# Kernel optimization log

Hardware: AMD Instinct MI355X
Metric: run time of the kernel (lower is better)

## Reference

```python
import jax, jax.numpy as jnp
import numpy as np

BATCH = 1048576
D_IN = 4        # d_in=3 spatial dims + 1 time dim
HID = 64
N_HID_STACK = 4  # hidden residual blocks after the first hidden layer
D_OUT = 3
BN_EPS = 1e-5


def _bn(x, gamma, beta):
    # BatchNorm1d in training mode: biased batch statistics over the batch axis
    mu = jnp.mean(x, axis=0)
    var = jnp.var(x, axis=0)
    return gamma * (x - mu) * jax.lax.rsqrt(var + BN_EPS) + beta


def setup_inputs() -> dict:
    key = jax.random.key(0)
    ks = jax.random.split(key, 8)
    s_in = 1.0 / np.sqrt(D_IN)
    s_h = 1.0 / np.sqrt(HID)
    return {
        "x": jax.random.normal(ks[0], (BATCH, D_IN), dtype=jnp.float32),
        "bn0_gamma": jnp.ones((D_IN,), jnp.float32),
        "bn0_beta": jnp.zeros((D_IN,), jnp.float32),
        "W0": jax.random.normal(ks[1], (D_IN, HID), jnp.float32) * s_in,
        "b0": jnp.zeros((HID,), jnp.float32),
        "gamma0": jnp.ones((HID,), jnp.float32),
        "beta0": jnp.zeros((HID,), jnp.float32),
        "W_hid": jax.random.normal(ks[2], (N_HID_STACK, HID, HID), jnp.float32) * s_h,
        "b_hid": jnp.zeros((N_HID_STACK, HID), jnp.float32),
        "gamma_hid": jnp.ones((N_HID_STACK, HID), jnp.float32),
        "beta_hid": jnp.zeros((N_HID_STACK, HID), jnp.float32),
        "Wout": jax.random.normal(ks[3], (HID, D_OUT), jnp.float32) * s_h,
        "bout": jnp.zeros((D_OUT,), jnp.float32),
    }


def reference(x, bn0_gamma, bn0_beta, W0, b0, gamma0, beta0,
              W_hid, b_hid, gamma_hid, beta_hid, Wout, bout):
    # Net.forward (u-network, single patch, batch_normalization=True, tanh):
    #   x = bn0(x)
    #   y = bn(act(Linear0(x)))                 (first hidden layer, no skip)
    #   y = bn_i(act(Linear_i(y))) + y          (residual hidden layers)
    #   y = Linear_out(y)
    h = _bn(x, bn0_gamma, bn0_beta)
    y = _bn(jnp.tanh(h @ W0 + b0), gamma0, beta0)

    def step(y, layer):
        W, b, g, be = layer
        return _bn(jnp.tanh(y @ W + b), g, be) + y, None

    y, _ = jax.lax.scan(step, y, (W_hid, b_hid, gamma_hid, beta_hid))
    return y @ Wout + bout
```

## Files before the change

### kernel.cpp

```cpp
#include <hip/hip_runtime.h>
#include <stdint.h>


#define NROWS 1048576
#define EPS 1e-5f
#define INV_B 9.5367431640625e-07f
#define LOG2E2 2.885390081777927f
#define BIGGRID 16384

typedef __attribute__((ext_vector_type(8))) short bfrag;
typedef __attribute__((ext_vector_type(4))) float facc;
typedef __attribute__((ext_vector_type(4))) float f4v;

__device__ __forceinline__ float bf2f(short s) {
  union { unsigned u; float f; } v;
  v.u = ((unsigned)(unsigned short)s) << 16;
  return v.f;
}
__device__ __forceinline__ short f2bf(float f) {
  union { float f; unsigned u; } v;
  v.f = f;
  unsigned r = v.u + 0x7FFFu + ((v.u >> 16) & 1u);
  return (short)(r >> 16);
}
__device__ __forceinline__ float tanh_fast(float x) {
  float e = __builtin_amdgcn_exp2f(x * LOG2E2);
  return 1.f - 2.f * __builtin_amdgcn_rcpf(e + 1.f);
}

template <int W>
__global__ __launch_bounds__(256) void k_reduce(const float* __restrict__ P,
                                                float* __restrict__ S,
                                                int rows_per_blk) {
  __shared__ float red[256];
  const int tid = threadIdx.x;
  const int col = tid % W;
  const int grp = tid / W;
  const int G = 256 / W;
  size_t r0 = (size_t)blockIdx.x * rows_per_blk;
  float s = 0.f;
  for (int r = grp; r < rows_per_blk; r += G) s += P[(r0 + r) * W + col];
  red[tid] = s;
  __syncthreads();
  if (tid < W) {
    float t = 0.f;
#pragma unroll 4
    for (int g = 0; g < G; ++g) t += red[g * W + tid];
    atomicAdd(&S[tid], t);
  }
}


__global__ __launch_bounds__(256) void k_stats_x(const float* __restrict__ x,
                                                 float* __restrict__ P) {
  __shared__ float red[4][8];
  const int tid = threadIdx.x;
  const int wave = tid >> 6;
  size_t base = (size_t)blockIdx.x * 1024 + tid;
  float s[4] = {0.f, 0.f, 0.f, 0.f}, q[4] = {0.f, 0.f, 0.f, 0.f};
#pragma unroll
  for (int it = 0; it < 4; ++it) {
    f4v v = *(const f4v*)(x + (base + (size_t)it * 256) * 4);
#pragma unroll
    for (int k = 0; k < 4; ++k) { s[k] += v[k]; q[k] = fmaf(v[k], v[k], q[k]); }
  }
#pragma unroll
  for (int off = 32; off > 0; off >>= 1) {
#pragma unroll
    for (int k = 0; k < 4; ++k) {
      s[k] += __shfl_xor(s[k], off);
      q[k] += __shfl_xor(q[k], off);
    }
  }
  if ((tid & 63) == 0) {
#pragma unroll
    for (int k = 0; k < 4; ++k) { red[wave][k] = s[k]; red[wave][4 + k] = q[k]; }
  }
  __syncthreads();
  if (tid < 8)
    P[blockIdx.x * 8 + tid] =
        red[0][tid] + red[1][tid] + red[2][tid] + red[3][tid];
}

__global__ __launch_bounds__(256) void k_stats_z1(
    const float* __restrict__ x, const float* __restrict__ bn0g,
    const float* __restrict__ bn0b, const float* __restrict__ W0,
    const float* __restrict__ b0, const float* __restrict__ sx,
    float* __restrict__ P) {
  __shared__ float red[2][4][64];
  const int tid = threadIdx.x;
  const int lane = tid & 63;
  const int wave = tid >> 6;
  int gw = blockIdx.x * 4 + wave;
  float sc[4], sh[4];
#pragma unroll
  for (int k = 0; k < 4; ++k) {
    float mean = sx[k] * INV_B;
    float var = fmaf(-mean, mean, sx[4 + k] * INV_B);
    float rs = rsqrtf(var + EPS);
    sc[k] = bn0g[k] * rs;
    sh[k] = fmaf(-sc[k], mean, bn0b[k]);
  }
  float w[4];
#pragma unroll
  for (int k = 0; k < 4; ++k) w[k] = W0[k * 64 + lane];
  float bj = b0[lane];
  float s = 0.f, q = 0.f;
  size_t r0 = (size_t)gw * 256;
  for (int r = 0; r < 256; ++r) {
    f4v xv = *(const f4v*)(x + (r0 + r) * 4);
    float acc = bj;
#pragma unroll
    for (int k = 0; k < 4; ++k)
      acc = fmaf(fmaf(xv[k], sc[k], sh[k]), w[k], acc);
    float z = tanh_fast(acc);
    s += z;
    q = fmaf(z, z, q);
  }
  red[0][wave][lane] = s;
  red[1][wave][lane] = q;
  __syncthreads();
  if (tid < 128) {
    int which = tid >> 6, c = tid & 63;
    P[blockIdx.x * 128 + tid] = red[which][0][c] + red[which][1][c] +
                                red[which][2][c] + red[which][3][c];
  }
}

__global__ __launch_bounds__(256) void k_prep(const float* __restrict__ Wh,
                                              short* __restrict__ WT) {
  int idx = blockIdx.x * 256 + threadIdx.x;
  int l = idx >> 12, rem = idx & 4095, k = rem >> 6, c = rem & 63;
  WT[l * 4096 + c * 64 + k] = f2bf(Wh[l * 4096 + k * 64 + c]);
}


__global__ __launch_bounds__(128) void k_first(
    const float* __restrict__ x, const float* __restrict__ bn0g,
    const float* __restrict__ bn0b, const float* __restrict__ W0,
    const float* __restrict__ b0, const float* __restrict__ gamma0,
    const float* __restrict__ beta0, const float* __restrict__ sx,
    const float* __restrict__ s1, const short* __restrict__ WTb,
    const float* __restrict__ bb, float* __restrict__ P,
    short* __restrict__ Y) {
  __shared__ __align__(16) float lds_x[64 * 4];
  __shared__ __align__(16) short lds_y[64 * 72];
  __shared__ float lds_st[128];

  const int tid = threadIdx.x;
  const int lane = tid & 63;
  const int wave = tid >> 6;
  const int l15 = lane & 15;
  const int q = lane >> 4;
  const int wr = wave * 32;
  const size_t r0 = (size_t)blockIdx.x * 64;

  f4v xp;
  if (lane < 32) xp = *(const f4v*)(x + (r0 + wr + lane) * 4);

  lds_st[tid] = 0.f;
  float sc0[4], sh0[4];
#pragma unroll
  for (int k = 0; k < 4; ++k) {
    float mean = sx[k] * INV_B;
    float var = fmaf(-mean, mean, sx[4 + k] * INV_B);
    float rs = rsqrtf(var + EPS);
    sc0[k] = bn0g[k] * rs;
    sh0[k] = fmaf(-sc0[k], mean, bn0b[k]);
  }
  float w0c[4];
#pragma unroll
  for (int k = 0; k < 4; ++k) w0c[k] = W0[k * 64 + lane];
  float b0c = b0[lane];
  float mean1 = s1[lane] * INV_B;
  float var1 = fmaf(-mean1, mean1, s1[64 + lane] * INV_B);
  float A1c = gamma0[lane] * rsqrtf(var1 + EPS);
  float B1c = fmaf(-A1c, mean1, beta0[lane]);
  if (lane < 32) *(f4v*)&lds_x[(wr + lane) * 4] = xp;
  __syncthreads();

  for (int e = 0; e < 32; ++e) {
    int row = wr + e;
    float acc = b0c;
#pragma unroll
    for (int k = 0; k < 4; ++k)
      acc = fmaf(fmaf(lds_x[row * 4 + k], sc0[k], sh0[k]), w0c[k], acc);
    float z = tanh_fast(acc);
    lds_y[row * 72 + lane] = f2bf(fmaf(A1c, z, B1c));
  }

  bfrag af[2][2];
#pragma unroll
  for (int mt = 0; mt < 2; ++mt)
#pragma unroll
    for (int kt = 0; kt < 2; ++kt) {
      af[mt][kt] =
          *(const bfrag*)&lds_y[(wr + mt * 16 + l15) * 72 + kt * 32 + q * 8];
      *(bfrag*)(Y + (r0 + wr + mt * 16 + l15) * 64 + kt * 32 + q * 8) =
          af[mt][kt];
    }
  float bbv[4];
  bfrag bwb[4][2];
#pragma unroll
  for (int nt = 0; nt < 4; ++nt) {
    bbv[nt] = bb[nt * 16 + l15];
#pragma unroll
    for (int kt = 0; kt < 2; ++kt)
      bwb[nt][kt] =
          *(const bfrag*)(WTb + (nt * 16 + l15) * 64 + kt * 32 + q * 8);
  }
  facc acc2[2][4];
#pragma unroll
  for (int mt = 0; mt < 2; ++mt)
#pragma unroll
    for (int nt = 0; nt < 4; ++nt) {
      acc2[mt][nt][0] = bbv[nt]; acc2[mt][nt][1] = bbv[nt];
      acc2[mt][nt][2] = bbv[nt]; acc2[mt][nt][3] = bbv[nt];
    }
#pragma unroll
  for (int mt = 0; mt < 2; ++mt)
#pragma unroll
    for (int nt = 0; nt < 4; ++nt)
#pragma unroll
      for (int kt = 0; kt < 2; ++kt)
        acc2[mt][nt] = __builtin_amdgcn_mfma_f32_16x16x32_bf16(
            af[mt][kt], bwb[nt][kt], acc2[mt][nt], 0, 0, 0);
  float sAcc[4], qAcc[4];
#pragma unroll
  for (int nt = 0; nt < 4; ++nt) {
    sAcc[nt] = 0.f;
    qAcc[nt] = 0.f;
#pragma unroll
    for (int mt = 0; mt < 2; ++mt)
#pragma unroll
      for (int i = 0; i < 4; ++i) {
        float z = tanh_fast(acc2[mt][nt][i]);
        sAcc[nt] += z;
        qAcc[nt] = fmaf(z, z, qAcc[nt]);
      }
    float s = sAcc[nt], ss = qAcc[nt];
    s += __shfl_xor(s, 16); s += __shfl_xor(s, 32);
    ss += __shfl_xor(ss, 16); ss += __shfl_xor(ss, 32);
    if (q == 0) {
      atomicAdd(&lds_st[nt * 16 + l15], s);
      atomicAdd(&lds_st[64 + nt * 16 + l15], ss);
    }
  }
  __syncthreads();
  P[(size_t)blockIdx.x * 128 + tid] = lds_st[tid];
}

__global__ __launch_bounds__(128) void k_mid(
    short* __restrict__ Y, const short* __restrict__ WTa,
    const float* __restrict__ ba, const float* __restrict__ ga,
    const float* __restrict__ bea, const float* __restrict__ sa,
    const short* __restrict__ WTb, const float* __restrict__ bb,
    float* __restrict__ P) {
  __shared__ __align__(16) short lds_y[64 * 72];
  __shared__ float lds_st[128];

  const int tid = threadIdx.x;
  const int lane = tid & 63;
  const int wave = tid >> 6;
  const int l15 = lane & 15;
  const int q = lane >> 4;
  const int wr = wave * 32;
  const size_t r0 = (size_t)blockIdx.x * 64;
  const int srow = lane >> 3;
  const int sc8 = (lane & 7) * 8;

  bfrag ld[4];
  {
    const size_t g = (r0 + wr + srow) * 64 + sc8;
#pragma unroll
    for (int it = 0; it < 4; ++it)
      ld[it] = *(const bfrag*)(Y + g + (size_t)it * 8 * 64);
  }

  lds_st[tid] = 0.f;
  float Av[4], Bv[4], bav[4];
#pragma unroll
  for (int nt = 0; nt < 4; ++nt) {
    int c = nt * 16 + l15;
    float mean = sa[c] * INV_B;
    float var = fmaf(-mean, mean, sa[64 + c] * INV_B);
    float A = ga[c] * rsqrtf(var + EPS);
    Av[nt] = A;
    Bv[nt] = fmaf(-A, mean, bea[c]);
    bav[nt] = ba[c];
  }
  bfrag bwa[4][2];
#pragma unroll
  for (int nt = 0; nt < 4; ++nt)
#pragma unroll
    for (int kt = 0; kt < 2; ++kt)
      bwa[nt][kt] =
          *(const bfrag*)(WTa + (nt * 16 + l15) * 64 + kt * 32 + q * 8);

#pragma unroll
  for (int it = 0; it < 4; ++it)
    *(bfrag*)&lds_y[(wr + it * 8 + srow) * 72 + sc8] = ld[it];
  __syncthreads();

  bfrag af[2][2];
#pragma unroll
  for (int mt = 0; mt < 2; ++mt)
#pragma unroll
    for (int kt = 0; kt < 2; ++kt)
      af[mt][kt] =
          *(const bfrag*)&lds_y[(wr + mt * 16 + l15) * 72 + kt * 32 + q * 8];
  facc acc[2][4];
#pragma unroll
  for (int mt = 0; mt < 2; ++mt)
#pragma unroll
    for (int nt = 0; nt < 4; ++nt) {
      acc[mt][nt][0] = bav[nt]; acc[mt][nt][1] = bav[nt];
      acc[mt][nt][2] = bav[nt]; acc[mt][nt][3] = bav[nt];
    }
#pragma unroll
  for (int mt = 0; mt < 2; ++mt)
#pragma unroll
    for (int nt = 0; nt < 4; ++nt)
#pragma unroll
      for (int kt = 0; kt < 2; ++kt)
        acc[mt][nt] = __builtin_amdgcn_mfma_f32_16x16x32_bf16(
            af[mt][kt], bwa[nt][kt], acc[mt][nt], 0, 0, 0);

#pragma unroll
  for (int mt = 0; mt < 2; ++mt)
#pragma unroll
    for (int nt = 0; nt < 4; ++nt) {
      int c = nt * 16 + l15;
      float A = Av[nt], Bc = Bv[nt];
#pragma unroll
      for (int i = 0; i < 4; ++i) {
        int rl = wr + mt * 16 + q * 4 + i;
        float z = tanh_fast(acc[mt][nt][i]);
        float yo = bf2f(lds_y[rl * 72 + c]);
        lds_y[rl * 72 + c] = f2bf(fmaf(A, z, Bc) + yo);
      }
    }

#pragma unroll
  for (int mt = 0; mt < 2; ++mt)
#pragma unroll
    for (int kt = 0; kt < 2; ++kt) {
      af[mt][kt] =
          *(const bfrag*)&lds_y[(wr + mt * 16 + l15) * 72 + kt * 32 + q * 8];
      *(bfrag*)(Y + (r0 + wr + mt * 16 + l15) * 64 + kt * 32 + q * 8) =
          af[mt][kt];
    }
  float bbv[4];
  bfrag bwb[4][2];
#pragma unroll
  for (int nt = 0; nt < 4; ++nt) {
    bbv[nt] = bb[nt * 16 + l15];
#pragma unroll
    for (int kt = 0; kt < 2; ++kt)
      bwb[nt][kt] =
          *(const bfrag*)(WTb + (nt * 16 + l15) * 64 + kt * 32 + q * 8);
  }
#pragma unroll
  for (int mt = 0; mt < 2; ++mt)
#pragma unroll
    for (int nt = 0; nt < 4; ++nt) {
      acc[mt][nt][0] = bbv[nt]; acc[mt][nt][1] = bbv[nt];
      acc[mt][nt][2] = bbv[nt]; acc[mt][nt][3] = bbv[nt];
    }
#pragma unroll
  for (int mt = 0; mt < 2; ++mt)
#pragma unroll
    for (int nt = 0; nt < 4; ++nt)
#pragma unroll
      for (int kt = 0; kt < 2; ++kt)
        acc[mt][nt] = __builtin_amdgcn_mfma_f32_16x16x32_bf16(
            af[mt][kt], bwb[nt][kt], acc[mt][nt], 0, 0, 0);
#pragma unroll
  for (int nt = 0; nt < 4; ++nt) {
    float s = 0.f, ss = 0.f;
#pragma unroll
    for (int mt = 0; mt < 2; ++mt)
#pragma unroll
      for (int i = 0; i < 4; ++i) {
        float z = tanh_fast(acc[mt][nt][i]);
        s += z;
        ss = fmaf(z, z, ss);
      }
    s += __shfl_xor(s, 16); s += __shfl_xor(s, 32);
    ss += __shfl_xor(ss, 16); ss += __shfl_xor(ss, 32);
    if (q == 0) {
      atomicAdd(&lds_st[nt * 16 + l15], s);
      atomicAdd(&lds_st[64 + nt * 16 + l15], ss);
    }
  }
  __syncthreads();
  P[(size_t)blockIdx.x * 128 + tid] = lds_st[tid];
}

__global__ __launch_bounds__(128) void k_last(
    const short* __restrict__ Y, const short* __restrict__ WTa,
    const float* __restrict__ ba, const float* __restrict__ ga,
    const float* __restrict__ bea, const float* __restrict__ sa,
    const float* __restrict__ Wout, const float* __restrict__ bout,
    float* __restrict__ out) {
  __shared__ __align__(16) short lds_y[64 * 72];
  __shared__ float lds_wo[192];

  const int tid = threadIdx.x;
  const int lane = tid & 63;
  const int wave = tid >> 6;
  const int l15 = lane & 15;
  const int q = lane >> 4;
  const int wr = wave * 32;
  const size_t r0 = (size_t)blockIdx.x * 64;
  const int srow = lane >> 3;
  const int sc8 = (lane & 7) * 8;

  bfrag ld[4];
  {
    const size_t g = (r0 + wr + srow) * 64 + sc8;
#pragma unroll
    for (int it = 0; it < 4; ++it)
      ld[it] = *(const bfrag*)(Y + g + (size_t)it * 8 * 64);
  }

  for (int i = tid; i < 192; i += 128) lds_wo[i] = Wout[i];
  float Av[4], Bv[4], bav[4];
#pragma unroll
  for (int nt = 0; nt < 4; ++nt) {
    int c = nt * 16 + l15;
    float mean = sa[c] * INV_B;
    float var = fmaf(-mean, mean, sa[64 + c] * INV_B);
    float A = ga[c] * rsqrtf(var + EPS);
    Av[nt] = A;
    Bv[nt] = fmaf(-A, mean, bea[c]);
    bav[nt] = ba[c];
  }
  bfrag bwa[4][2];
#pragma unroll
  for (int nt = 0; nt < 4; ++nt)
#pragma unroll
    for (int kt = 0; kt < 2; ++kt)
      bwa[nt][kt] =
          *(const bfrag*)(WTa + (nt * 16 + l15) * 64 + kt * 32 + q * 8);
  float bo0 = bout[0], bo1 = bout[1], bo2 = bout[2];

#pragma unroll
  for (int it = 0; it < 4; ++it)
    *(bfrag*)&lds_y[(wr + it * 8 + srow) * 72 + sc8] = ld[it];
  __syncthreads();

  bfrag af[2][2];
#pragma unroll
  for (int mt = 0; mt < 2; ++mt)
#pragma unroll
    for (int kt = 0; kt < 2; ++kt)
      af[mt][kt] =
          *(const bfrag*)&lds_y[(wr + mt * 16 + l15) * 72 + kt * 32 + q * 8];
  facc acc[2][4];
#pragma unroll
  for (int mt = 0; mt < 2; ++mt)
#pragma unroll
    for (int nt = 0; nt < 4; ++nt) {
      acc[mt][nt][0] = bav[nt]; acc[mt][nt][1] = bav[nt];
      acc[mt][nt][2] = bav[nt]; acc[mt][nt][3] = bav[nt];
    }
#pragma unroll
  for (int mt = 0; mt < 2; ++mt)
#pragma unroll
    for (int nt = 0; nt < 4; ++nt)
#pragma unroll
      for (int kt = 0; kt < 2; ++kt)
        acc[mt][nt] = __builtin_amdgcn_mfma_f32_16x16x32_bf16(
            af[mt][kt], bwa[nt][kt], acc[mt][nt], 0, 0, 0);
#pragma unroll
  for (int mt = 0; mt < 2; ++mt)
#pragma unroll
    for (int nt = 0; nt < 4; ++nt) {
      int c = nt * 16 + l15;
      float A = Av[nt], Bc = Bv[nt];
#pragma unroll
      for (int i = 0; i < 4; ++i) {
        int rl = wr + mt * 16 + q * 4 + i;
        float z = tanh_fast(acc[mt][nt][i]);
        float yo = bf2f(lds_y[rl * 72 + c]);
        lds_y[rl * 72 + c] = f2bf(fmaf(A, z, Bc) + yo);
      }
    }

  {
    int row = wr + (lane >> 1);
    int cb = (lane & 1) * 32;
    float o0 = 0.f, o1 = 0.f, o2 = 0.f;
#pragma unroll
    for (int jc = 0; jc < 4; ++jc) {
      bfrag v = *(const bfrag*)&lds_y[row * 72 + cb + jc * 8];
#pragma unroll
      for (int j = 0; j < 8; ++j) {
        float f = bf2f(v[j]);
        int jj = cb + jc * 8 + j;
        o0 = fmaf(f, lds_wo[jj * 3 + 0], o0);
        o1 = fmaf(f, lds_wo[jj * 3 + 1], o1);
        o2 = fmaf(f, lds_wo[jj * 3 + 2], o2);
      }
    }
    o0 += __shfl_xor(o0, 1);
    o1 += __shfl_xor(o1, 1);
    o2 += __shfl_xor(o2, 1);
    if ((lane & 1) == 0) {
      size_t ro = (r0 + row) * 3;
      out[ro] = o0 + bo0;
      out[ro + 1] = o1 + bo1;
      out[ro + 2] = o2 + bo2;
    }
  }
}

extern "C" void kernel_launch(void* const* d_in, const int* in_sizes, int n_in,
                              void* d_out, int out_size, void* d_ws,
                              size_t ws_size, hipStream_t stream) {
  (void)in_sizes; (void)n_in; (void)out_size; (void)ws_size;
  const float* x = (const float*)d_in[0];
  const float* bn0g = (const float*)d_in[1];
  const float* bn0b = (const float*)d_in[2];
  const float* W0 = (const float*)d_in[3];
  const float* b0 = (const float*)d_in[4];
  const float* gamma0 = (const float*)d_in[5];
  const float* beta0 = (const float*)d_in[6];
  const float* Wh = (const float*)d_in[7];
  const float* bh = (const float*)d_in[8];
  const float* gh = (const float*)d_in[9];
  const float* beh = (const float*)d_in[10];
  const float* Wout = (const float*)d_in[11];
  const float* bout = (const float*)d_in[12];
  float* out = (float*)d_out;

  char* ws = (char*)d_ws;
  short* Y = (short*)ws;
  const size_t YB = (size_t)NROWS * 64 * 2;
  float* stats = (float*)(ws + YB);
  float* Sx = stats;
  float* S1 = stats + 8;
  float* S2 = stats + 136;
  float* S3 = stats + 264;
  float* S4 = stats + 392;
  float* S5 = stats + 520;
  short* WT = (short*)(ws + YB + 4096);
  float* P = (float*)(ws + YB + 4096 + 32768);

  hipMemsetAsync(stats, 0, 648 * sizeof(float), stream);
  k_prep<<<64, 256, 0, stream>>>(Wh, WT);
  k_stats_x<<<1024, 256, 0, stream>>>(x, P);
  k_reduce<8><<<8, 256, 0, stream>>>(P, Sx, 128);
  k_stats_z1<<<1024, 256, 0, stream>>>(x, bn0g, bn0b, W0, b0, Sx, P);
  k_reduce<128><<<8, 256, 0, stream>>>(P, S1, 128);
  k_first<<<BIGGRID, 128, 0, stream>>>(x, bn0g, bn0b, W0, b0, gamma0, beta0,
                                       Sx, S1, WT, bh, P, Y);
  k_reduce<128><<<128, 256, 0, stream>>>(P, S2, 128);
  k_mid<<<BIGGRID, 128, 0, stream>>>(Y, WT, bh, gh, beh, S2, WT + 4096,
                                     bh + 64, P);
  k_reduce<128><<<128, 256, 0, stream>>>(P, S3, 128);
  k_mid<<<BIGGRID, 128, 0, stream>>>(Y, WT + 4096, bh + 64, gh + 64, beh + 64,
                                     S3, WT + 2 * 4096, bh + 128, P);
  k_reduce<128><<<128, 256, 0, stream>>>(P, S4, 128);
  k_mid<<<BIGGRID, 128, 0, stream>>>(Y, WT + 2 * 4096, bh + 128, gh + 128,
                                     beh + 128, S4, WT + 3 * 4096, bh + 192, P);
  k_reduce<128><<<128, 256, 0, stream>>>(P, S5, 128);
  k_last<<<BIGGRID, 128, 0, stream>>>(Y, WT + 3 * 4096, bh + 192, gh + 192,
                                      beh + 192, S5, Wout, bout, out);
}
```

Baseline: 562.4 us.

## Replace per-block partials and reduce kernels with padded global atomics; widen blocks

Drops the separate reduction kernels by having each block atomically add its BN partial sums directly into padded global accumulators, spaced 16 floats apart to avoid contention on one cache line. Blocks grow to 256 threads covering 128 rows. Mid and last kernels now load activation fragments straight from global memory and recover the residual via an identity-matrix MFMA rather than staging through LDS. The last kernel computes the output projection directly from MFMA accumulators with shuffles. The risk is heavy atomic traffic from 8192 blocks onto the same addresses, plus extra MFMA work for the identity trick.

```diff
diff --git a/kernel.cpp b/kernel.cpp
--- a/kernel.cpp
+++ b/kernel.cpp
@@ -6,7 +6,7 @@
 #define EPS 1e-5f
 #define INV_B 9.5367431640625e-07f
 #define LOG2E2 2.885390081777927f
-#define BIGGRID 16384
+#define BIGGRID 8192
 
 typedef __attribute__((ext_vector_type(8))) short bfrag;
 typedef __attribute__((ext_vector_type(4))) float facc;
@@ -28,31 +28,17 @@
   return 1.f - 2.f * __builtin_amdgcn_rcpf(e + 1.f);
 }
 
-template <int W>
-__global__ __launch_bounds__(256) void k_reduce(const float* __restrict__ P,
-                                                float* __restrict__ S,
-                                                int rows_per_blk) {
-  __shared__ float red[256];
-  const int tid = threadIdx.x;
-  const int col = tid % W;
-  const int grp = tid / W;
-  const int G = 256 / W;
-  size_t r0 = (size_t)blockIdx.x * rows_per_blk;
-  float s = 0.f;
-  for (int r = grp; r < rows_per_blk; r += G) s += P[(r0 + r) * W + col];
-  red[tid] = s;
-  __syncthreads();
-  if (tid < W) {
-    float t = 0.f;
-#pragma unroll 4
-    for (int g = 0; g < G; ++g) t += red[g * W + tid];
-    atomicAdd(&S[tid], t);
-  }
+__device__ __forceinline__ bfrag make_ident(int l15, int q, int p) {
+  bfrag r;
+  const short one = (short)0x3F80;
+#pragma unroll
+  for (int j = 0; j < 8; ++j) r[j] = (q * 8 + j == l15 + 16 * p) ? one : 0;
+  return r;
 }
 
 
 __global__ __launch_bounds__(256) void k_stats_x(const float* __restrict__ x,
-                                                 float* __restrict__ P) {
+                                                 float* __restrict__ Sx) {
   __shared__ float red[4][8];
   const int tid = threadIdx.x;
   const int wave = tid >> 6;
@@ -78,15 +64,15 @@
   }
   __syncthreads();
   if (tid < 8)
-    P[blockIdx.x * 8 + tid] =
-        red[0][tid] + red[1][tid] + red[2][tid] + red[3][tid];
+    atomicAdd(&Sx[tid * 16],
+              red[0][tid] + red[1][tid] + red[2][tid] + red[3][tid]);
 }
 
 __global__ __launch_bounds__(256) void k_stats_z1(
     const float* __restrict__ x, const float* __restrict__ bn0g,
     const float* __restrict__ bn0b, const float* __restrict__ W0,
     const float* __restrict__ b0, const float* __restrict__ sx,
-    float* __restrict__ P) {
+    float* __restrict__ S1) {
   __shared__ float red[2][4][64];
   const int tid = threadIdx.x;
   const int lane = tid & 63;
@@ -95,8 +81,8 @@
   float sc[4], sh[4];
 #pragma unroll
   for (int k = 0; k < 4; ++k) {
-    float mean = sx[k] * INV_B;
-    float var = fmaf(-mean, mean, sx[4 + k] * INV_B);
+    float mean = sx[k * 16] * INV_B;
+    float var = fmaf(-mean, mean, sx[(4 + k) * 16] * INV_B);
     float rs = rsqrtf(var + EPS);
     sc[k] = bn0g[k] * rs;
     sh[k] = fmaf(-sc[k], mean, bn0b[k]);
@@ -122,8 +108,8 @@
   __syncthreads();
   if (tid < 128) {
     int which = tid >> 6, c = tid & 63;
-    P[blockIdx.x * 128 + tid] = red[which][0][c] + red[which][1][c] +
-                                red[which][2][c] + red[which][3][c];
+    atomicAdd(&S1[tid * 16], red[which][0][c] + red[which][1][c] +
+                                 red[which][2][c] + red[which][3][c]);
   }
 }
 
@@ -135,17 +121,17 @@
 }
 
 
-__global__ __launch_bounds__(128) void k_first(
+__global__ __launch_bounds__(256) void k_first(
     const float* __restrict__ x, const float* __restrict__ bn0g,
     const float* __restrict__ bn0b, const float* __restrict__ W0,
     const float* __restrict__ b0, const float* __restrict__ gamma0,
     const float* __restrict__ beta0, const float* __restrict__ sx,
     const float* __restrict__ s1, const short* __restrict__ WTb,
-    const float* __restrict__ bb, float* __restrict__ P,
+    const float* __restrict__ bb, float* __restrict__ Sb,
     short* __restrict__ Y) {
-  __shared__ __align__(16) float lds_x[64 * 4];
-  __shared__ __align__(16) short lds_y[64 * 72];
-  __shared__ float lds_st[128];
+  __shared__ __align__(16) float lds_x[128 * 4];
+  __shared__ __align__(16) short ly[128 * 72];
+  __shared__ float lds_st[4][128];
 
   const int tid = threadIdx.x;
   const int lane = tid & 63;
@@ -153,17 +139,16 @@
   const int l15 = lane & 15;
   const int q = lane >> 4;
   const int wr = wave * 32;
-  const size_t r0 = (size_t)blockIdx.x * 64;
+  const size_t r0 = (size_t)blockIdx.x * 128;
 
   f4v xp;
   if (lane < 32) xp = *(const f4v*)(x + (r0 + wr + lane) * 4);
 
-  lds_st[tid] = 0.f;
   float sc0[4], sh0[4];
 #pragma unroll
   for (int k = 0; k < 4; ++k) {
-    float mean = sx[k] * INV_B;
-    float var = fmaf(-mean, mean, sx[4 + k] * INV_B);
+    float mean = sx[k * 16] * INV_B;
+    float var = fmaf(-mean, mean, sx[(4 + k) * 16] * INV_B);
     float rs = rsqrtf(var + EPS);
     sc0[k] = bn0g[k] * rs;
     sh0[k] = fmaf(-sc0[k], mean, bn0b[k]);
@@ -172,12 +157,12 @@
 #pragma unroll
   for (int k = 0; k < 4; ++k) w0c[k] = W0[k * 64 + lane];
   float b0c = b0[lane];
-  float mean1 = s1[lane] * INV_B;
-  float var1 = fmaf(-mean1, mean1, s1[64 + lane] * INV_B);
+  float mean1 = s1[lane * 16] * INV_B;
+  float var1 = fmaf(-mean1, mean1, s1[(64 + lane) * 16] * INV_B);
   float A1c = gamma0[lane] * rsqrtf(var1 + EPS);
   float B1c = fmaf(-A1c, mean1, beta0[lane]);
+
   if (lane < 32) *(f4v*)&lds_x[(wr + lane) * 4] = xp;
-  __syncthreads();
 
   for (int e = 0; e < 32; ++e) {
     int row = wr + e;
@@ -186,7 +171,7 @@
     for (int k = 0; k < 4; ++k)
       acc = fmaf(fmaf(lds_x[row * 4 + k], sc0[k], sh0[k]), w0c[k], acc);
     float z = tanh_fast(acc);
-    lds_y[row * 72 + lane] = f2bf(fmaf(A1c, z, B1c));
+    ly[row * 72 + lane] = f2bf(fmaf(A1c, z, B1c));
   }
 
   bfrag af[2][2];
@@ -195,7 +180,7 @@
 #pragma unroll
     for (int kt = 0; kt < 2; ++kt) {
       af[mt][kt] =
-          *(const bfrag*)&lds_y[(wr + mt * 16 + l15) * 72 + kt * 32 + q * 8];
+          *(const bfrag*)&ly[(wr + mt * 16 + l15) * 72 + kt * 32 + q * 8];
       *(bfrag*)(Y + (r0 + wr + mt * 16 + l15) * 64 + kt * 32 + q * 8) =
           af[mt][kt];
     }
@@ -225,39 +210,38 @@
       for (int kt = 0; kt < 2; ++kt)
         acc2[mt][nt] = __builtin_amdgcn_mfma_f32_16x16x32_bf16(
             af[mt][kt], bwb[nt][kt], acc2[mt][nt], 0, 0, 0);
-  float sAcc[4], qAcc[4];
 #pragma unroll
   for (int nt = 0; nt < 4; ++nt) {
-    sAcc[nt] = 0.f;
-    qAcc[nt] = 0.f;
+    float s = 0.f, ss = 0.f;
 #pragma unroll
     for (int mt = 0; mt < 2; ++mt)
 #pragma unroll
       for (int i = 0; i < 4; ++i) {
         float z = tanh_fast(acc2[mt][nt][i]);
-        sAcc[nt] += z;
-        qAcc[nt] = fmaf(z, z, qAcc[nt]);
+        s += z;
+        ss = fmaf(z, z, ss);
       }
-    float s = sAcc[nt], ss = qAcc[nt];
     s += __shfl_xor(s, 16); s += __shfl_xor(s, 32);
     ss += __shfl_xor(ss, 16); ss += __shfl_xor(ss, 32);
     if (q == 0) {
-      atomicAdd(&lds_st[nt * 16 + l15], s);
-      atomicAdd(&lds_st[64 + nt * 16 + l15], ss);
+      lds_st[wave][nt * 16 + l15] = s;
+      lds_st[wave][64 + nt * 16 + l15] = ss;
     }
   }
   __syncthreads();
-  P[(size_t)blockIdx.x * 128 + tid] = lds_st[tid];
-}
-
-__global__ __launch_bounds__(128) void k_mid(
+  if (tid < 128)
+    atomicAdd(&Sb[tid * 16], lds_st[0][tid] + lds_st[1][tid] + lds_st[2][tid] +
+                                 lds_st[3][tid]);
+}
+
+__global__ __launch_bounds__(256) void k_mid(
     short* __restrict__ Y, const short* __restrict__ WTa,
     const float* __restrict__ ba, const float* __restrict__ ga,
     const float* __restrict__ bea, const float* __restrict__ sa,
     const short* __restrict__ WTb, const float* __restrict__ bb,
-    float* __restrict__ P) {
-  __shared__ __align__(16) short lds_y[64 * 72];
-  __shared__ float lds_st[128];
+    float* __restrict__ Sb) {
+  __shared__ __align__(16) short ly[128 * 72];
+  __shared__ float lds_st[4][128];
 
   const int tid = threadIdx.x;
   const int lane = tid & 63;
@@ -265,25 +249,22 @@
   const int l15 = lane & 15;
   const int q = lane >> 4;
   const int wr = wave * 32;
-  const size_t r0 = (size_t)blockIdx.x * 64;
-  const int srow = lane >> 3;
-  const int sc8 = (lane & 7) * 8;
-
-  bfrag ld[4];
-  {
-    const size_t g = (r0 + wr + srow) * 64 + sc8;
-#pragma unroll
-    for (int it = 0; it < 4; ++it)
-      ld[it] = *(const bfrag*)(Y + g + (size_t)it * 8 * 64);
-  }
-
-  lds_st[tid] = 0.f;
+  const size_t r0 = (size_t)blockIdx.x * 128;
+
+  bfrag af[2][2];
+#pragma unroll
+  for (int mt = 0; mt < 2; ++mt)
+#pragma unroll
+    for (int kt = 0; kt < 2; ++kt)
+      af[mt][kt] =
+          *(const bfrag*)(Y + (r0 + wr + mt * 16 + l15) * 64 + kt * 32 + q * 8);
+
   float Av[4], Bv[4], bav[4];
 #pragma unroll
   for (int nt = 0; nt < 4; ++nt) {
     int c = nt * 16 + l15;
-    float mean = sa[c] * INV_B;
-    float var = fmaf(-mean, mean, sa[64 + c] * INV_B);
+    float mean = sa[c * 16] * INV_B;
+    float var = fmaf(-mean, mean, sa[(64 + c) * 16] * INV_B);
     float A = ga[c] * rsqrtf(var + EPS);
     Av[nt] = A;
     Bv[nt] = fmaf(-A, mean, bea[c]);
@@ -296,38 +277,27 @@
     for (int kt = 0; kt < 2; ++kt)
       bwa[nt][kt] =
           *(const bfrag*)(WTa + (nt * 16 + l15) * 64 + kt * 32 + q * 8);
-
-#pragma unroll
-  for (int it = 0; it < 4; ++it)
-    *(bfrag*)&lds_y[(wr + it * 8 + srow) * 72 + sc8] = ld[it];
-  __syncthreads();
-
-  bfrag af[2][2];
-#pragma unroll
-  for (int mt = 0; mt < 2; ++mt)
-#pragma unroll
-    for (int kt = 0; kt < 2; ++kt)
-      af[mt][kt] =
-          *(const bfrag*)&lds_y[(wr + mt * 16 + l15) * 72 + kt * 32 + q * 8];
-  facc acc[2][4];
-#pragma unroll
-  for (int mt = 0; mt < 2; ++mt)
-#pragma unroll
-    for (int nt = 0; nt < 4; ++nt) {
-      acc[mt][nt][0] = bav[nt]; acc[mt][nt][1] = bav[nt];
-      acc[mt][nt][2] = bav[nt]; acc[mt][nt][3] = bav[nt];
-    }
-#pragma unroll
-  for (int mt = 0; mt < 2; ++mt)
-#pragma unroll
-    for (int nt = 0; nt < 4; ++nt)
+  const bfrag bI0 = make_ident(l15, q, 0);
+  const bfrag bI1 = make_ident(l15, q, 1);
+
+#pragma unroll
+  for (int mt = 0; mt < 2; ++mt) {
+    facc acc[4], yC[4];
+#pragma unroll
+    for (int nt = 0; nt < 4; ++nt) {
+      acc[nt][0] = bav[nt]; acc[nt][1] = bav[nt];
+      acc[nt][2] = bav[nt]; acc[nt][3] = bav[nt];
+      yC[nt][0] = 0.f; yC[nt][1] = 0.f; yC[nt][2] = 0.f; yC[nt][3] = 0.f;
+    }
+#pragma unroll
+    for (int nt = 0; nt < 4; ++nt) {
 #pragma unroll
       for (int kt = 0; kt < 2; ++kt)
-        acc[mt][nt] = __builtin_amdgcn_mfma_f32_16x16x32_bf16(
-            af[mt][kt], bwa[nt][kt], acc[mt][nt], 0, 0, 0);
-
-#pragma unroll
-  for (int mt = 0; mt < 2; ++mt)
+        acc[nt] = __builtin_amdgcn_mfma_f32_16x16x32_bf16(
+            af[mt][kt], bwa[nt][kt], acc[nt], 0, 0, 0);
+      yC[nt] = __builtin_amdgcn_mfma_f32_16x16x32_bf16(
+          af[mt][nt >> 1], (nt & 1) ? bI1 : bI0, yC[nt], 0, 0, 0);
+    }
 #pragma unroll
     for (int nt = 0; nt < 4; ++nt) {
       int c = nt * 16 + l15;
@@ -335,18 +305,18 @@
 #pragma unroll
       for (int i = 0; i < 4; ++i) {
         int rl = wr + mt * 16 + q * 4 + i;
-        float z = tanh_fast(acc[mt][nt][i]);
-        float yo = bf2f(lds_y[rl * 72 + c]);
-        lds_y[rl * 72 + c] = f2bf(fmaf(A, z, Bc) + yo);
+        float z = tanh_fast(acc[nt][i]);
+        ly[rl * 72 + c] = f2bf(fmaf(A, z, Bc) + yC[nt][i]);
       }
     }
+  }
 
 #pragma unroll
   for (int mt = 0; mt < 2; ++mt)
 #pragma unroll
     for (int kt = 0; kt < 2; ++kt) {
       af[mt][kt] =
-          *(const bfrag*)&lds_y[(wr + mt * 16 + l15) * 72 + kt * 32 + q * 8];
+          *(const bfrag*)&ly[(wr + mt * 16 + l15) * 72 + kt * 32 + q * 8];
       *(bfrag*)(Y + (r0 + wr + mt * 16 + l15) * 64 + kt * 32 + q * 8) =
           af[mt][kt];
     }
@@ -360,12 +330,13 @@
       bwb[nt][kt] =
           *(const bfrag*)(WTb + (nt * 16 + l15) * 64 + kt * 32 + q * 8);
   }
-#pragma unroll
-  for (int mt = 0; mt < 2; ++mt)
-#pragma unroll
-    for (int nt = 0; nt < 4; ++nt) {
-      acc[mt][nt][0] = bbv[nt]; acc[mt][nt][1] = bbv[nt];
-      acc[mt][nt][2] = bbv[nt]; acc[mt][nt][3] = bbv[nt];
+  facc acc2[2][4];
+#pragma unroll
+  for (int mt = 0; mt < 2; ++mt)
+#pragma unroll
+    for (int nt = 0; nt < 4; ++nt) {
+      acc2[mt][nt][0] = bbv[nt]; acc2[mt][nt][1] = bbv[nt];
+      acc2[mt][nt][2] = bbv[nt]; acc2[mt][nt][3] = bbv[nt];
     }
 #pragma unroll
   for (int mt = 0; mt < 2; ++mt)
@@ -373,8 +344,8 @@
     for (int nt = 0; nt < 4; ++nt)
 #pragma unroll
       for (int kt = 0; kt < 2; ++kt)
-        acc[mt][nt] = __builtin_amdgcn_mfma_f32_16x16x32_bf16(
-            af[mt][kt], bwb[nt][kt], acc[mt][nt], 0, 0, 0);
+        acc2[mt][nt] = __builtin_amdgcn_mfma_f32_16x16x32_bf16(
+            af[mt][kt], bwb[nt][kt], acc2[mt][nt], 0, 0, 0);
 #pragma unroll
   for (int nt = 0; nt < 4; ++nt) {
     float s = 0.f, ss = 0.f;
@@ -382,59 +353,57 @@
     for (int mt = 0; mt < 2; ++mt)
 #pragma unroll
       for (int i = 0; i < 4; ++i) {
-        float z = tanh_fast(acc[mt][nt][i]);
+        float z = tanh_fast(acc2[mt][nt][i]);
         s += z;
         ss = fmaf(z, z, ss);
       }
     s += __shfl_xor(s, 16); s += __shfl_xor(s, 32);
     ss += __shfl_xor(ss, 16); ss += __shfl_xor(ss, 32);
     if (q == 0) {
-      atomicAdd(&lds_st[nt * 16 + l15], s);
-      atomicAdd(&lds_st[64 + nt * 16 + l15], ss);
+      lds_st[wave][nt * 16 + l15] = s;
+      lds_st[wave][64 + nt * 16 + l15] = ss;
     }
   }
   __syncthreads();
-  P[(size_t)blockIdx.x * 128 + tid] = lds_st[tid];
-}
-
-__global__ __launch_bounds__(128) void k_last(
+  if (tid < 128)
+    atomicAdd(&Sb[tid * 16], lds_st[0][tid] + lds_st[1][tid] + lds_st[2][tid] +
+                                 lds_st[3][tid]);
+}
+
+__global__ __launch_bounds__(256) void k_last(
     const short* __restrict__ Y, const short* __restrict__ WTa,
     const float* __restrict__ ba, const float* __restrict__ ga,
     const float* __restrict__ bea, const float* __restrict__ sa,
     const float* __restrict__ Wout, const float* __restrict__ bout,
     float* __restrict__ out) {
-  __shared__ __align__(16) short lds_y[64 * 72];
-  __shared__ float lds_wo[192];
-
   const int tid = threadIdx.x;
   const int lane = tid & 63;
   const int wave = tid >> 6;
   const int l15 = lane & 15;
   const int q = lane >> 4;
   const int wr = wave * 32;
-  const size_t r0 = (size_t)blockIdx.x * 64;
-  const int srow = lane >> 3;
-  const int sc8 = (lane & 7) * 8;
-
-  bfrag ld[4];
-  {
-    const size_t g = (r0 + wr + srow) * 64 + sc8;
-#pragma unroll
-    for (int it = 0; it < 4; ++it)
-      ld[it] = *(const bfrag*)(Y + g + (size_t)it * 8 * 64);
-  }
-
-  for (int i = tid; i < 192; i += 128) lds_wo[i] = Wout[i];
-  float Av[4], Bv[4], bav[4];
+  const size_t r0 = (size_t)blockIdx.x * 128;
+
+  bfrag af[2][2];
+#pragma unroll
+  for (int mt = 0; mt < 2; ++mt)
+#pragma unroll
+    for (int kt = 0; kt < 2; ++kt)
+      af[mt][kt] =
+          *(const bfrag*)(Y + (r0 + wr + mt * 16 + l15) * 64 + kt * 32 + q * 8);
+
+  float Av[4], Bv[4], bav[4], wo[4][3];
 #pragma unroll
   for (int nt = 0; nt < 4; ++nt) {
     int c = nt * 16 + l15;
-    float mean = sa[c] * INV_B;
-    float var = fmaf(-mean, mean, sa[64 + c] * INV_B);
+    float mean = sa[c * 16] * INV_B;
+    float var = fmaf(-mean, mean, sa[(64 + c) * 16] * INV_B);
     float A = ga[c] * rsqrtf(var + EPS);
     Av[nt] = A;
     Bv[nt] = fmaf(-A, mean, bea[c]);
     bav[nt] = ba[c];
+#pragma unroll
+    for (int o = 0; o < 3; ++o) wo[nt][o] = Wout[c * 3 + o];
   }
   bfrag bwa[4][2];
 #pragma unroll
@@ -443,75 +412,51 @@
     for (int kt = 0; kt < 2; ++kt)
       bwa[nt][kt] =
           *(const bfrag*)(WTa + (nt * 16 + l15) * 64 + kt * 32 + q * 8);
+  const bfrag bI0 = make_ident(l15, q, 0);
+  const bfrag bI1 = make_ident(l15, q, 1);
   float bo0 = bout[0], bo1 = bout[1], bo2 = bout[2];
 
 #pragma unroll
-  for (int it = 0; it < 4; ++it)
-    *(bfrag*)&lds_y[(wr + it * 8 + srow) * 72 + sc8] = ld[it];
-  __syncthreads();
-
-  bfrag af[2][2];
-#pragma unroll
-  for (int mt = 0; mt < 2; ++mt)
-#pragma unroll
-    for (int kt = 0; kt < 2; ++kt)
-      af[mt][kt] =
-          *(const bfrag*)&lds_y[(wr + mt * 16 + l15) * 72 + kt * 32 + q * 8];
-  facc acc[2][4];
-#pragma unroll
-  for (int mt = 0; mt < 2; ++mt)
-#pragma unroll
-    for (int nt = 0; nt < 4; ++nt) {
-      acc[mt][nt][0] = bav[nt]; acc[mt][nt][1] = bav[nt];
-      acc[mt][nt][2] = bav[nt]; acc[mt][nt][3] = bav[nt];
-    }
-#pragma unroll
-  for (int mt = 0; mt < 2; ++mt)
-#pragma unroll
-    for (int nt = 0; nt < 4; ++nt)
+  for (int mt = 0; mt < 2; ++mt) {
+    facc acc[4], yC[4];
+#pragma unroll
+    for (int nt = 0; nt < 4; ++nt) {
+      acc[nt][0] = bav[nt]; acc[nt][1] = bav[nt];
+      acc[nt][2] = bav[nt]; acc[nt][3] = bav[nt];
+      yC[nt][0] = 0.f; yC[nt][1] = 0.f; yC[nt][2] = 0.f; yC[nt][3] = 0.f;
+    }
+#pragma unroll
+    for (int nt = 0; nt < 4; ++nt) {
 #pragma unroll
       for (int kt = 0; kt < 2; ++kt)
-        acc[mt][nt] = __builtin_amdgcn_mfma_f32_16x16x32_bf16(
-            af[mt][kt], bwa[nt][kt], acc[mt][nt], 0, 0, 0);
-#pragma unroll
-  for (int mt = 0; mt < 2; ++mt)
-#pragma unroll
-    for (int nt = 0; nt < 4; ++nt) {
-      int c = nt * 16 + l15;
-      float A = Av[nt], Bc = Bv[nt];
-#pragma unroll
-      for (int i = 0; i < 4; ++i) {
-        int rl = wr + mt * 16 + q * 4 + i;
-        float z = tanh_fast(acc[mt][nt][i]);
-        float yo = bf2f(lds_y[rl * 72 + c]);
-        lds_y[rl * 72 + c] = f2bf(fmaf(A, z, Bc) + yo);
+        acc[nt] = __builtin_amdgcn_mfma_f32_16x16x32_bf16(
+            af[mt][kt], bwa[nt][kt], acc[nt], 0, 0, 0);
+      yC[nt] = __builtin_amdgcn_mfma_f32_16x16x32_bf16(
+          af[mt][nt >> 1], (nt & 1) ? bI1 : bI0, yC[nt], 0, 0, 0);
+    }
+#pragma unroll
+    for (int i = 0; i < 4; ++i) {
+      float o0 = 0.f, o1 = 0.f, o2 = 0.f;
+#pragma unroll
+      for (int nt = 0; nt < 4; ++nt) {
+        float z = tanh_fast(acc[nt][i]);
+        float yn = bf2f(f2bf(fmaf(Av[nt], z, Bv[nt]) + yC[nt][i]));
+        o0 = fmaf(yn, wo[nt][0], o0);
+        o1 = fmaf(yn, wo[nt][1], o1);
+        o2 = fmaf(yn, wo[nt][2], o2);
       }
-    }
-
-  {
-    int row = wr + (lane >> 1);
-    int cb = (lane & 1) * 32;
-    float o0 = 0.f, o1 = 0.f, o2 = 0.f;
-#pragma unroll
-    for (int jc = 0; jc < 4; ++jc) {
-      bfrag v = *(const bfrag*)&lds_y[row * 72 + cb + jc * 8];
-#pragma unroll
-      for (int j = 0; j < 8; ++j) {
-        float f = bf2f(v[j]);
-        int jj = cb + jc * 8 + j;
-        o0 = fmaf(f, lds_wo[jj * 3 + 0], o0);
-        o1 = fmaf(f, lds_wo[jj * 3 + 1], o1);
-        o2 = fmaf(f, lds_wo[jj * 3 + 2], o2);
+#pragma unroll
+      for (int off = 1; off < 16; off <<= 1) {
+        o0 += __shfl_xor(o0, off);
+        o1 += __shfl_xor(o1, off);
+        o2 += __shfl_xor(o2, off);
       }
-    }
-    o0 += __shfl_xor(o0, 1);
-    o1 += __shfl_xor(o1, 1);
-    o2 += __shfl_xor(o2, 1);
-    if ((lane & 1) == 0) {
-      size_t ro = (r0 + row) * 3;
-      out[ro] = o0 + bo0;
-      out[ro + 1] = o1 + bo1;
-      out[ro + 2] = o2 + bo2;
+      if (l15 == 0) {
+        size_t ro = (r0 + wr + mt * 16 + q * 4 + i) * 3;
+        out[ro] = o0 + bo0;
+        out[ro + 1] = o1 + bo1;
+        out[ro + 2] = o2 + bo2;
+      }
     }
   }
 }
@@ -540,32 +485,27 @@
   const size_t YB = (size_t)NROWS * 64 * 2;
   float* stats = (float*)(ws + YB);
   float* Sx = stats;
-  float* S1 = stats + 8;
-  float* S2 = stats + 136;
-  float* S3 = stats + 264;
-  float* S4 = stats + 392;
-  float* S5 = stats + 520;
-  short* WT = (short*)(ws + YB + 4096);
-  float* P = (float*)(ws + YB + 4096 + 32768);
-
-  hipMemsetAsync(stats, 0, 648 * sizeof(float), stream);
+  float* S1 = stats + 128;
+  float* S2 = S1 + 2048;
+  float* S3 = S2 + 2048;
+  float* S4 = S3 + 2048;
+  float* S5 = S4 + 2048;
+  const size_t STATS_FLOATS = 128 + 5 * 2048;
+  short* WT = (short*)(ws + YB + STATS_FLOATS * sizeof(float) + 256);
+
+  hipMemsetAsync(stats, 0, STATS_FLOATS * sizeof(float), stream);
   k_prep<<<64, 256, 0, stream>>>(Wh, WT);
-  k_stats_x<<<1024, 256, 0, stream>>>(x, P);
-  k_reduce<8><<<8, 256, 0, stream>>>(P, Sx, 128);
-  k_stats_z1<<<1024, 256, 0, stream>>>(x, bn0g, bn0b, W0, b0, Sx, P);
-  k_reduce<128><<<8, 256, 0, stream>>>(P, S1, 128);
-  k_first<<<BIGGRID, 128, 0, stream>>>(x, bn0g, bn0b, W0, b0, gamma0, beta0,
-                                       Sx, S1, WT, bh, P, Y);
-  k_reduce<128><<<128, 256, 0, stream>>>(P, S2, 128);
-  k_mid<<<BIGGRID, 128, 0, stream>>>(Y, WT, bh, gh, beh, S2, WT + 4096,
-                                     bh + 64, P);
-  k_reduce<128><<<128, 256, 0, stream>>>(P, S3, 128);
-  k_mid<<<BIGGRID, 128, 0, stream>>>(Y, WT + 4096, bh + 64, gh + 64, beh + 64,
-                                     S3, WT + 2 * 4096, bh + 128, P);
-  k_reduce<128><<<128, 256, 0, stream>>>(P, S4, 128);
-  k_mid<<<BIGGRID, 128, 0, stream>>>(Y, WT + 2 * 4096, bh + 128, gh + 128,
-                                     beh + 128, S4, WT + 3 * 4096, bh + 192, P);
-  k_reduce<128><<<128, 256, 0, stream>>>(P, S5, 128);
-  k_last<<<BIGGRID, 128, 0, stream>>>(Y, WT + 3 * 4096, bh + 192, gh + 192,
+  k_stats_x<<<1024, 256, 0, stream>>>(x, Sx);
+  k_stats_z1<<<1024, 256, 0, stream>>>(x, bn0g, bn0b, W0, b0, Sx, S1);
+  k_first<<<BIGGRID, 256, 0, stream>>>(x, bn0g, bn0b, W0, b0, gamma0, beta0,
+                                       Sx, S1, WT, bh, S2, Y);
+  k_mid<<<BIGGRID, 256, 0, stream>>>(Y, WT, bh, gh, beh, S2, WT + 4096,
+                                     bh + 64, S3);
+  k_mid<<<BIGGRID, 256, 0, stream>>>(Y, WT + 4096, bh + 64, gh + 64, beh + 64,
+                                     S3, WT + 2 * 4096, bh + 128, S4);
+  k_mid<<<BIGGRID, 256, 0, stream>>>(Y, WT + 2 * 4096, bh + 128, gh + 128,
+                                     beh + 128, S4, WT + 3 * 4096, bh + 192,
+                                     S5);
+  k_last<<<BIGGRID, 256, 0, stream>>>(Y, WT + 3 * 4096, bh + 192, gh + 192,
                                       beh + 192, S5, Wout, bout, out);
 }
```

After: 1.182 ms. 2.1x slower.
